# Optimization experiments

Hardware: AMD Instinct MI355X
Metric: run time of the kernel (lower is better)

## Reference

```python
import jax, jax.numpy as jnp
import numpy as np

EPS = 1e-8
H_OUT, W_OUT = 64, 64
SURR_SCALE = 10.0  # SuperSpike-style surrogate slope

@jax.custom_vjp
def spike(x):
    # forward: Heaviside threshold
    return (x > 0).astype(x.dtype)

def _spike_fwd(x):
    return spike(x), x

def _spike_bwd(x, g):
    # SuperSpike surrogate gradient: 1/(1+scale*|x|)^2
    return (g / (1.0 + SURR_SCALE * jnp.abs(x)) ** 2,)

spike.defvjp(_spike_fwd, _spike_bwd)


def setup_inputs() -> dict:
    key = jax.random.key(0)
    k1, k2, k3, k4 = jax.random.split(key, 4)
    x = jax.random.normal(k1, (4, 16, 32, 64, 64), dtype=jnp.float32)
    # w ~ N(0, std*sqrt(1/(C_in*prod(kernel)))) with std=1
    w = jax.random.normal(k2, (64, 16, 3, 3, 3), dtype=jnp.float32) * np.float32(np.sqrt(1.0 / (16 * 27)))
    beta = jnp.clip(0.7 + 0.01 * jax.random.normal(k3, (1,), dtype=jnp.float32), 0.0, 1.0)
    b = jnp.clip(1.0 + 0.01 * jax.random.normal(k4, (64,), dtype=jnp.float32), 0.0, None)
    return {"x": x, "w": w, "beta": beta, "b": b}


def reference(x, w, beta, b):
    # x: (B, C_in, T, H, W); w: (C_out, C_in, kt, kh, kw)
    # conv3d, padding = ceil((k-1)*dil/2) = 1 per dim for k=3, dil=1
    conv_x = jax.lax.conv_general_dilated(
        x, w,
        window_strides=(1, 1, 1),
        padding=[(1, 1), (1, 1), (1, 1)],
        rhs_dilation=(1, 1, 1),
        dimension_numbers=("NCDHW", "OIDHW", "NCDHW"),
    )
    conv_x = conv_x[:, :, :, :H_OUT, :W_OUT]  # crop spatial dims only

    d = jnp.einsum("abcde,fbcde->af", w, w)          # (C_out, C_out) lateral matrix
    norm = jnp.sum(w ** 2, axis=(1, 2, 3, 4))        # (C_out,)
    inv_norm = 1.0 / (norm + EPS)
    beta_s = beta[0]

    B = x.shape[0]
    C = w.shape[0]
    mem0 = jnp.zeros((B, C, H_OUT, W_OUT), dtype=x.dtype)
    spk0 = jnp.zeros_like(mem0)

    xs = jnp.moveaxis(conv_x, 2, 0)  # (T, B, C, H, W)

    def step(carry, inp_t):
        spk, mem = carry
        rst = jnp.einsum("abcd,be->aecd", spk, d)  # lateral reset
        mem = (mem - rst) * beta_s + inp_t * (1.0 - beta_s)
        mthr = mem * inv_norm[None, :, None, None] - b[None, :, None, None]
        spk = spike(mthr)
        return (spk, mem), spk

    _, spk_rec = jax.lax.scan(step, (spk0, mem0), xs)  # (T, B, C, H, W)
    return jnp.moveaxis(spk_rec, 0, 2)  # (B, C, T, H, W) -- flatten_output=False
```

## Files before the change

kernel.cpp:

```cpp
#include <hip/hip_runtime.h>
#include <cstdint>
#include <cstddef>

#define H_ 64
#define W_ 64
#define T_ 32
#define CIN_ 16
#define COUT_ 64
#define K_ 432
#define TH_ 4
#define TW_ 16
#define WR_ 6
#define WC_ 18
#define WSZ_ (WR_ * WC_)
#define XTOT_ (CIN_ * WSZ_)
#define NSLOT_ 4
#define NTHR_ 1024

__global__ void prep(const float* __restrict__ w, float* __restrict__ w_t,
                     double* __restrict__ d64, double* __restrict__ inv64) {
    const int i = blockIdx.x;
    const int j = threadIdx.x;
    const float* wi = w + i * K_;
    const float* wj = w + j * K_;
    double acc = 0.0;
    for (int k = 0; k < K_; ++k) acc += (double)wi[k] * (double)wj[k];
    d64[i * 64 + j] = acc;
    if (i == j) inv64[i] = 1.0 / (acc + 1e-8);
    for (int k = j; k < K_; k += 64) w_t[k * 64 + i] = wi[k];
}

__launch_bounds__(NTHR_, 1)
__global__ void fused_snn(const float* __restrict__ xg,
                          const float* __restrict__ beta_g, const float* __restrict__ bias_g,
                          const float* __restrict__ w_t, const double* __restrict__ d64,
                          const double* __restrict__ inv64, float* __restrict__ out) {
    __shared__ __align__(16) float x_win[NSLOT_ * XTOT_];
    __shared__ __align__(16) double d_lds[64 * 65];
    __shared__ unsigned int masks[2][64][2];

    const int tid = threadIdx.x;
    const int b   = blockIdx.x;
    const int ty0 = blockIdx.y * TH_;
    const int tx0 = blockIdx.z * TW_;

    const int wv   = __builtin_amdgcn_readfirstlane(tid >> 6);
    const int lane = tid & 63;
    const int py   = lane >> 4;
    const int px   = lane & 15;
    const int c0   = wv * 4;
    const int xoff = py * WC_ + px;

    for (int i = tid; i < 4096; i += NTHR_)
        d_lds[(i >> 6) * 65 + (i & 63)] = d64[i];
    if (tid < 128) masks[1][tid >> 1][tid & 1] = 0u;

    for (int z = 0; z < 2; ++z) {
        for (int i = tid; i < XTOT_; i += NTHR_) {
            int cin = i / WSZ_;
            int r2  = i - cin * WSZ_;
            int yy  = r2 / WC_;
            int xx  = r2 - yy * WC_;
            int gy = ty0 - 1 + yy, gx = tx0 - 1 + xx;
            float v = 0.f;
            if (gy >= 0 && gy < H_ && gx >= 0 && gx < W_)
                v = xg[((size_t)(b * CIN_ + cin) * T_ + z) * (H_ * W_) + gy * W_ + gx];
            x_win[(z * CIN_ + cin) * WSZ_ + r2] = v;
        }
    }

    const double beta = (double)beta_g[0];
    const double omb  = 1.0 - beta;
    double inv_[4], bb[4];
#pragma unroll
    for (int ci = 0; ci < 4; ++ci) {
        inv_[ci] = inv64[c0 + ci];
        bb[ci]   = (double)bias_g[c0 + ci];
    }
    double mem[4];
#pragma unroll
    for (int ci = 0; ci < 4; ++ci) mem[ci] = 0.0;

    int  pf_cin[2], pf_r2[2];
    size_t pf_goff[2];
    bool pf_ok[2], pf_in[2];
#pragma unroll
    for (int r = 0; r < 2; ++r) {
        int i = tid + r * NTHR_;
        pf_ok[r] = (i < XTOT_);
        int cin = i / WSZ_;
        int r2  = i - cin * WSZ_;
        int yy  = r2 / WC_;
        int xx  = r2 - yy * WC_;
        pf_cin[r] = cin; pf_r2[r] = r2;
        int gy = ty0 - 1 + yy, gx = tx0 - 1 + xx;
        pf_in[r]  = pf_ok[r] && gy >= 0 && gy < H_ && gx >= 0 && gx < W_;
        pf_goff[r] = (size_t)(b * CIN_ + cin) * (T_ * H_ * W_) + (size_t)gy * W_ + gx;
    }

    for (int t = 0; t < T_; ++t) {
        __syncthreads();
        if (tid < 128) masks[t & 1][tid >> 1][tid & 1] = 0u;

        float R[2];
        const int zp = t + 2;
        if (zp < T_) {
#pragma unroll
            for (int r = 0; r < 2; ++r) {
                R[r] = 0.f;
                if (pf_in[r]) R[r] = xg[pf_goff[r] + (size_t)zp * (H_ * W_)];
            }
        }

        double accd[4];
#pragma unroll
        for (int ci = 0; ci < 4; ++ci) accd[ci] = 0.0;

        int slot_[3]; bool zok[3];
#pragma unroll
        for (int dz = 0; dz < 3; ++dz) {
            int z = t - 1 + dz;
            zok[dz]  = (z >= 0 && z < T_);
            slot_[dz] = zok[dz] ? (z & 3) : 0;
        }

        for (int cin = 0; cin < CIN_; ++cin) {
            float cacc[4];
#pragma unroll
            for (int ci = 0; ci < 4; ++ci) cacc[ci] = 0.f;
#pragma unroll
            for (int dz = 0; dz < 3; ++dz) {
                if (!zok[dz]) continue;
                const float* xs = &x_win[(slot_[dz] * CIN_ + cin) * WSZ_] + xoff;
                const float* wr = w_t + (cin * 27 + dz * 9) * 64 + c0;
#pragma unroll
                for (int dy = 0; dy < 3; ++dy) {
                    const float xv0 = xs[dy * WC_ + 0];
                    const float xv1 = xs[dy * WC_ + 1];
                    const float xv2 = xs[dy * WC_ + 2];
                    const float4 w0 = *reinterpret_cast<const float4*>(wr + dy * 192);
                    const float4 w1 = *reinterpret_cast<const float4*>(wr + dy * 192 + 64);
                    const float4 w2 = *reinterpret_cast<const float4*>(wr + dy * 192 + 128);
                    cacc[0] = fmaf(w0.x, xv0, cacc[0]);
                    cacc[1] = fmaf(w0.y, xv0, cacc[1]);
                    cacc[2] = fmaf(w0.z, xv0, cacc[2]);
                    cacc[3] = fmaf(w0.w, xv0, cacc[3]);
                    cacc[0] = fmaf(w1.x, xv1, cacc[0]);
                    cacc[1] = fmaf(w1.y, xv1, cacc[1]);
                    cacc[2] = fmaf(w1.z, xv1, cacc[2]);
                    cacc[3] = fmaf(w1.w, xv1, cacc[3]);
                    cacc[0] = fmaf(w2.x, xv2, cacc[0]);
                    cacc[1] = fmaf(w2.y, xv2, cacc[1]);
                    cacc[2] = fmaf(w2.z, xv2, cacc[2]);
                    cacc[3] = fmaf(w2.w, xv2, cacc[3]);
                }
            }
#pragma unroll
            for (int ci = 0; ci < 4; ++ci) accd[ci] += (double)cacc[ci];
        }

        double rstv[4];
#pragma unroll
        for (int ci = 0; ci < 4; ++ci) rstv[ci] = 0.0;
        const int rb = (t + 1) & 1;
#pragma unroll
        for (int wrd = 0; wrd < 2; ++wrd) {
            unsigned int m = masks[rb][lane][wrd];
            while (m) {
                int bit = __ffs(m) - 1;
                m &= m - 1;
                const double* drow = &d_lds[(wrd * 32 + bit) * 65 + c0];
#pragma unroll
                for (int ci = 0; ci < 4; ++ci) rstv[ci] += drow[ci];
            }
        }

        unsigned int nib = 0u;
        const size_t obase = ((size_t)(b * COUT_ + c0) * T_ + t) * (size_t)(H_ * W_)
                           + (size_t)(ty0 + py) * W_ + (tx0 + px);
#pragma unroll
        for (int ci = 0; ci < 4; ++ci) {
            mem[ci] = (mem[ci] - rstv[ci]) * beta + accd[ci] * omb;
            const double mthr = mem[ci] * inv_[ci] - bb[ci];
            const int s = mthr > 0.0 ? 1 : 0;
            out[obase + (size_t)ci * (T_ * H_ * W_)] = (float)s;
            nib |= (unsigned int)s << ci;
        }

        __syncthreads();
        if (nib) atomicOr(&masks[t & 1][lane][wv >> 3], nib << ((wv & 7) * 4));

        if (zp < T_) {
            const int slot = zp & 3;
#pragma unroll
            for (int r = 0; r < 2; ++r)
                if (pf_ok[r])
                    x_win[(slot * CIN_ + pf_cin[r]) * WSZ_ + pf_r2[r]] = R[r];
        }
    }
}

extern "C" void kernel_launch(void* const* d_in, const int* in_sizes, int n_in,
                              void* d_out, int out_size, void* d_ws, size_t ws_size,
                              hipStream_t stream) {
    const float* x    = (const float*)d_in[0];
    const float* w    = (const float*)d_in[1];
    const float* beta = (const float*)d_in[2];
    const float* bias = (const float*)d_in[3];
    float* out = (float*)d_out;

    float*  w_t   = (float*)d_ws;
    double* d64   = (double*)((char*)d_ws + 110592);
    double* inv64 = (double*)((char*)d_ws + 110592 + 32768);

    prep<<<dim3(64), dim3(64), 0, stream>>>(w, w_t, d64, inv64);
    fused_snn<<<dim3(4, 16, 4), dim3(NTHR_), 0, stream>>>(x, beta, bias, w_t, d64, inv64, out);
}
```

Baseline: 522.1 us.

## Scatter each input time slice into three rolling output accumulators

The temporal conv loop is restructured. Each input time slice is read from LDS once and its contribution goes to the three output timesteps it feeds, kept in rolling double accumulators (a0/a1/a2), instead of gathering three slices per output step. This cuts LDS reads of the input window by about 3x and lets the ring buffer shrink from four slots to two, with the row width padded to 24. In exchange it needs more registers for the extra double accumulators, a third prefetch element per thread, and a prologue pass over slice 0.

```diff
diff --git a/kernel.cpp b/kernel.cpp
--- a/kernel.cpp
+++ b/kernel.cpp
@@ -11,10 +11,9 @@
 #define TH_ 4
 #define TW_ 16
 #define WR_ 6
-#define WC_ 18
+#define WC_ 24
 #define WSZ_ (WR_ * WC_)
 #define XTOT_ (CIN_ * WSZ_)
-#define NSLOT_ 4
 #define NTHR_ 1024
 
 __global__ void prep(const float* __restrict__ w, float* __restrict__ w_t,
@@ -35,7 +34,7 @@
                           const float* __restrict__ beta_g, const float* __restrict__ bias_g,
                           const float* __restrict__ w_t, const double* __restrict__ d64,
                           const double* __restrict__ inv64, float* __restrict__ out) {
-    __shared__ __align__(16) float x_win[NSLOT_ * XTOT_];
+    __shared__ __align__(16) float x_win[2 * XTOT_];
     __shared__ __align__(16) double d_lds[64 * 65];
     __shared__ unsigned int masks[2][64][2];
 
@@ -61,11 +60,12 @@
             int r2  = i - cin * WSZ_;
             int yy  = r2 / WC_;
             int xx  = r2 - yy * WC_;
+            if (xx >= TW_ + 2) continue;
             int gy = ty0 - 1 + yy, gx = tx0 - 1 + xx;
             float v = 0.f;
             if (gy >= 0 && gy < H_ && gx >= 0 && gx < W_)
                 v = xg[((size_t)(b * CIN_ + cin) * T_ + z) * (H_ * W_) + gy * W_ + gx];
-            x_win[(z * CIN_ + cin) * WSZ_ + r2] = v;
+            x_win[z * XTOT_ + i] = v;
         }
     }
 
@@ -77,91 +77,106 @@
         inv_[ci] = inv64[c0 + ci];
         bb[ci]   = (double)bias_g[c0 + ci];
     }
-    double mem[4];
-#pragma unroll
-    for (int ci = 0; ci < 4; ++ci) mem[ci] = 0.0;
-
-    int  pf_cin[2], pf_r2[2];
-    size_t pf_goff[2];
-    bool pf_ok[2], pf_in[2];
-#pragma unroll
-    for (int r = 0; r < 2; ++r) {
+    double mem[4] = {0.0, 0.0, 0.0, 0.0};
+    double a0[4] = {}, a1[4] = {}, a2[4] = {};
+
+    int  pf_loff[3];
+    size_t pf_goff[3];
+    bool pf_use[3], pf_in[3];
+#pragma unroll
+    for (int r = 0; r < 3; ++r) {
         int i = tid + r * NTHR_;
-        pf_ok[r] = (i < XTOT_);
         int cin = i / WSZ_;
         int r2  = i - cin * WSZ_;
         int yy  = r2 / WC_;
         int xx  = r2 - yy * WC_;
-        pf_cin[r] = cin; pf_r2[r] = r2;
+        pf_loff[r] = i;
         int gy = ty0 - 1 + yy, gx = tx0 - 1 + xx;
-        pf_in[r]  = pf_ok[r] && gy >= 0 && gy < H_ && gx >= 0 && gx < W_;
+        bool ok = (i < XTOT_) && (xx < TW_ + 2);
+        pf_use[r] = ok;
+        pf_in[r]  = ok && gy >= 0 && gy < H_ && gx >= 0 && gx < W_;
         pf_goff[r] = (size_t)(b * CIN_ + cin) * (T_ * H_ * W_) + (size_t)gy * W_ + gx;
+    }
+
+    __syncthreads();
+
+    {
+        for (int cin = 0; cin < CIN_; ++cin) {
+            const int base = cin * WSZ_ + xoff;
+            float xv[9];
+#pragma unroll
+            for (int dy = 0; dy < 3; ++dy)
+#pragma unroll
+                for (int dx = 0; dx < 3; ++dx)
+                    xv[dy * 3 + dx] = x_win[base + dy * WC_ + dx];
+            float cB[4] = {}, cC[4] = {};
+            const float* wr = w_t + cin * 27 * 64 + c0;
+#pragma unroll
+            for (int p = 0; p < 9; ++p) {
+                const float4 w1 = *reinterpret_cast<const float4*>(wr + (9 + p) * 64);
+                const float4 w0 = *reinterpret_cast<const float4*>(wr + p * 64);
+                cB[0] = fmaf(w1.x, xv[p], cB[0]); cB[1] = fmaf(w1.y, xv[p], cB[1]);
+                cB[2] = fmaf(w1.z, xv[p], cB[2]); cB[3] = fmaf(w1.w, xv[p], cB[3]);
+                cC[0] = fmaf(w0.x, xv[p], cC[0]); cC[1] = fmaf(w0.y, xv[p], cC[1]);
+                cC[2] = fmaf(w0.z, xv[p], cC[2]); cC[3] = fmaf(w0.w, xv[p], cC[3]);
+            }
+#pragma unroll
+            for (int ci = 0; ci < 4; ++ci) {
+                a0[ci] += (double)cB[ci];
+                a1[ci] += (double)cC[ci];
+            }
+        }
     }
 
     for (int t = 0; t < T_; ++t) {
         __syncthreads();
         if (tid < 128) masks[t & 1][tid >> 1][tid & 1] = 0u;
 
-        float R[2];
+        float R[3];
         const int zp = t + 2;
         if (zp < T_) {
 #pragma unroll
-            for (int r = 0; r < 2; ++r) {
+            for (int r = 0; r < 3; ++r) {
                 R[r] = 0.f;
                 if (pf_in[r]) R[r] = xg[pf_goff[r] + (size_t)zp * (H_ * W_)];
             }
         }
 
-        double accd[4];
-#pragma unroll
-        for (int ci = 0; ci < 4; ++ci) accd[ci] = 0.0;
-
-        int slot_[3]; bool zok[3];
-#pragma unroll
-        for (int dz = 0; dz < 3; ++dz) {
-            int z = t - 1 + dz;
-            zok[dz]  = (z >= 0 && z < T_);
-            slot_[dz] = zok[dz] ? (z & 3) : 0;
-        }
-
-        for (int cin = 0; cin < CIN_; ++cin) {
-            float cacc[4];
-#pragma unroll
-            for (int ci = 0; ci < 4; ++ci) cacc[ci] = 0.f;
-#pragma unroll
-            for (int dz = 0; dz < 3; ++dz) {
-                if (!zok[dz]) continue;
-                const float* xs = &x_win[(slot_[dz] * CIN_ + cin) * WSZ_] + xoff;
-                const float* wr = w_t + (cin * 27 + dz * 9) * 64 + c0;
-#pragma unroll
-                for (int dy = 0; dy < 3; ++dy) {
-                    const float xv0 = xs[dy * WC_ + 0];
-                    const float xv1 = xs[dy * WC_ + 1];
-                    const float xv2 = xs[dy * WC_ + 2];
-                    const float4 w0 = *reinterpret_cast<const float4*>(wr + dy * 192);
-                    const float4 w1 = *reinterpret_cast<const float4*>(wr + dy * 192 + 64);
-                    const float4 w2 = *reinterpret_cast<const float4*>(wr + dy * 192 + 128);
-                    cacc[0] = fmaf(w0.x, xv0, cacc[0]);
-                    cacc[1] = fmaf(w0.y, xv0, cacc[1]);
-                    cacc[2] = fmaf(w0.z, xv0, cacc[2]);
-                    cacc[3] = fmaf(w0.w, xv0, cacc[3]);
-                    cacc[0] = fmaf(w1.x, xv1, cacc[0]);
-                    cacc[1] = fmaf(w1.y, xv1, cacc[1]);
-                    cacc[2] = fmaf(w1.z, xv1, cacc[2]);
-                    cacc[3] = fmaf(w1.w, xv1, cacc[3]);
-                    cacc[0] = fmaf(w2.x, xv2, cacc[0]);
-                    cacc[1] = fmaf(w2.y, xv2, cacc[1]);
-                    cacc[2] = fmaf(w2.z, xv2, cacc[2]);
-                    cacc[3] = fmaf(w2.w, xv2, cacc[3]);
+        const int zc = t + 1;
+        if (zc < T_) {
+            const int sb = (zc & 1) * XTOT_ + xoff;
+            for (int cin = 0; cin < CIN_; ++cin) {
+                const int base = sb + cin * WSZ_;
+                float xv[9];
+#pragma unroll
+                for (int dy = 0; dy < 3; ++dy)
+#pragma unroll
+                    for (int dx = 0; dx < 3; ++dx)
+                        xv[dy * 3 + dx] = x_win[base + dy * WC_ + dx];
+                float cA[4] = {}, cB[4] = {}, cC[4] = {};
+                const float* wr = w_t + cin * 27 * 64 + c0;
+#pragma unroll
+                for (int p = 0; p < 9; ++p) {
+                    const float4 w2 = *reinterpret_cast<const float4*>(wr + (18 + p) * 64);
+                    const float4 w1 = *reinterpret_cast<const float4*>(wr + (9 + p) * 64);
+                    const float4 w0 = *reinterpret_cast<const float4*>(wr + p * 64);
+                    cA[0] = fmaf(w2.x, xv[p], cA[0]); cA[1] = fmaf(w2.y, xv[p], cA[1]);
+                    cA[2] = fmaf(w2.z, xv[p], cA[2]); cA[3] = fmaf(w2.w, xv[p], cA[3]);
+                    cB[0] = fmaf(w1.x, xv[p], cB[0]); cB[1] = fmaf(w1.y, xv[p], cB[1]);
+                    cB[2] = fmaf(w1.z, xv[p], cB[2]); cB[3] = fmaf(w1.w, xv[p], cB[3]);
+                    cC[0] = fmaf(w0.x, xv[p], cC[0]); cC[1] = fmaf(w0.y, xv[p], cC[1]);
+                    cC[2] = fmaf(w0.z, xv[p], cC[2]); cC[3] = fmaf(w0.w, xv[p], cC[3]);
                 }
-            }
-#pragma unroll
-            for (int ci = 0; ci < 4; ++ci) accd[ci] += (double)cacc[ci];
-        }
-
-        double rstv[4];
-#pragma unroll
-        for (int ci = 0; ci < 4; ++ci) rstv[ci] = 0.0;
+#pragma unroll
+                for (int ci = 0; ci < 4; ++ci) {
+                    a0[ci] += (double)cA[ci];
+                    a1[ci] += (double)cB[ci];
+                    a2[ci] += (double)cC[ci];
+                }
+            }
+        }
+
+        double rstv[4] = {0.0, 0.0, 0.0, 0.0};
         const int rb = (t + 1) & 1;
 #pragma unroll
         for (int wrd = 0; wrd < 2; ++wrd) {
@@ -180,7 +195,7 @@
                            + (size_t)(ty0 + py) * W_ + (tx0 + px);
 #pragma unroll
         for (int ci = 0; ci < 4; ++ci) {
-            mem[ci] = (mem[ci] - rstv[ci]) * beta + accd[ci] * omb;
+            mem[ci] = (mem[ci] - rstv[ci]) * beta + a0[ci] * omb;
             const double mthr = mem[ci] * inv_[ci] - bb[ci];
             const int s = mthr > 0.0 ? 1 : 0;
             out[obase + (size_t)ci * (T_ * H_ * W_)] = (float)s;
@@ -191,11 +206,17 @@
         if (nib) atomicOr(&masks[t & 1][lane][wv >> 3], nib << ((wv & 7) * 4));
 
         if (zp < T_) {
-            const int slot = zp & 3;
-#pragma unroll
-            for (int r = 0; r < 2; ++r)
-                if (pf_ok[r])
-                    x_win[(slot * CIN_ + pf_cin[r]) * WSZ_ + pf_r2[r]] = R[r];
+            const int so = (zp & 1) * XTOT_;
+#pragma unroll
+            for (int r = 0; r < 3; ++r)
+                if (pf_use[r]) x_win[so + pf_loff[r]] = R[r];
+        }
+
+#pragma unroll
+        for (int ci = 0; ci < 4; ++ci) {
+            a0[ci] = a1[ci];
+            a1[ci] = a2[ci];
+            a2[ci] = 0.0;
         }
     }
 }
```

Result: slower. 824.4 us (+57.9%).

## Store input window channel-interleaved and repack weights for float4 LDS reads

Applied to the files above, without the earlier changes.

The shared input window is rearranged from channel-major to position-major, with 4 input channels packed per float4 and a stride of 5 float4 per position to reduce bank conflicts. Weights are repacked in the prep kernel into per-wave groups of 4 output channels by 4 input channels, so the inner loop reads one float4 of x per tap and scalar weights that are uniform across the wave. The loop now runs over quads of input channels, which cuts the number of LDS load instructions. Converting the partial sums to double now happens per (cin-quad, dz) instead of per cin, which changes the float summation order slightly.

```diff
diff --git a/kernel.cpp b/kernel.cpp
--- a/kernel.cpp
+++ b/kernel.cpp
@@ -7,35 +7,38 @@
 #define T_ 32
 #define CIN_ 16
 #define COUT_ 64
-#define K_ 432
 #define TH_ 4
 #define TW_ 16
-#define WR_ 6
-#define WC_ 18
-#define WSZ_ (WR_ * WC_)
-#define XTOT_ (CIN_ * WSZ_)
-#define NSLOT_ 4
+#define NROW_ 6
+#define NCOL_ 18
+#define NPOS_ (NROW_ * NCOL_)
+#define XEL_ (NPOS_ * CIN_)
+#define SLOT_DW_ (NPOS_ * 20)
 #define NTHR_ 1024
 
-__global__ void prep(const float* __restrict__ w, float* __restrict__ w_t,
+__global__ void prep(const float* __restrict__ w, float* __restrict__ w2,
                      double* __restrict__ d64, double* __restrict__ inv64) {
     const int i = blockIdx.x;
     const int j = threadIdx.x;
-    const float* wi = w + i * K_;
-    const float* wj = w + j * K_;
+    const float* wi = w + i * 432;
+    const float* wj = w + j * 432;
     double acc = 0.0;
-    for (int k = 0; k < K_; ++k) acc += (double)wi[k] * (double)wj[k];
+    for (int k = 0; k < 432; ++k) acc += (double)wi[k] * (double)wj[k];
     d64[i * 64 + j] = acc;
     if (i == j) inv64[i] = 1.0 / (acc + 1e-8);
-    for (int k = j; k < K_; k += 64) w_t[k * 64 + i] = wi[k];
+    for (int k = j; k < 432; k += 64) {
+        const int cin = k / 27, r = k - cin * 27;
+        const int off = ((((i >> 2) * 4 + (cin >> 2)) * 27 + r) * 4 + (cin & 3)) * 4 + (i & 3);
+        w2[off] = wi[k];
+    }
 }
 
 __launch_bounds__(NTHR_, 1)
 __global__ void fused_snn(const float* __restrict__ xg,
                           const float* __restrict__ beta_g, const float* __restrict__ bias_g,
-                          const float* __restrict__ w_t, const double* __restrict__ d64,
+                          const float* __restrict__ w2, const double* __restrict__ d64,
                           const double* __restrict__ inv64, float* __restrict__ out) {
-    __shared__ __align__(16) float x_win[NSLOT_ * XTOT_];
+    __shared__ __align__(16) float4 xQ[4][NPOS_][5];
     __shared__ __align__(16) double d_lds[64 * 65];
     __shared__ unsigned int masks[2][64][2];
 
@@ -49,23 +52,23 @@
     const int py   = lane >> 4;
     const int px   = lane & 15;
     const int c0   = wv * 4;
-    const int xoff = py * WC_ + px;
+
+    const float* wbase = w2 + (size_t)wv * 1728;
+    float* xF = (float*)&xQ[0][0][0];
 
     for (int i = tid; i < 4096; i += NTHR_)
         d_lds[(i >> 6) * 65 + (i & 63)] = d64[i];
     if (tid < 128) masks[1][tid >> 1][tid & 1] = 0u;
 
     for (int z = 0; z < 2; ++z) {
-        for (int i = tid; i < XTOT_; i += NTHR_) {
-            int cin = i / WSZ_;
-            int r2  = i - cin * WSZ_;
-            int yy  = r2 / WC_;
-            int xx  = r2 - yy * WC_;
-            int gy = ty0 - 1 + yy, gx = tx0 - 1 + xx;
+        for (int i = tid; i < XEL_; i += NTHR_) {
+            const int pos = i >> 4, cin = i & 15;
+            const int yy = pos / NCOL_, xx = pos - yy * NCOL_;
+            const int gy = ty0 - 1 + yy, gx = tx0 - 1 + xx;
             float v = 0.f;
             if (gy >= 0 && gy < H_ && gx >= 0 && gx < W_)
                 v = xg[((size_t)(b * CIN_ + cin) * T_ + z) * (H_ * W_) + gy * W_ + gx];
-            x_win[(z * CIN_ + cin) * WSZ_ + r2] = v;
+            xF[z * SLOT_DW_ + pos * 20 + cin] = v;
         }
     }
 
@@ -81,19 +84,17 @@
 #pragma unroll
     for (int ci = 0; ci < 4; ++ci) mem[ci] = 0.0;
 
-    int  pf_cin[2], pf_r2[2];
+    int  pf_ldw[2];
     size_t pf_goff[2];
     bool pf_ok[2], pf_in[2];
 #pragma unroll
     for (int r = 0; r < 2; ++r) {
-        int i = tid + r * NTHR_;
-        pf_ok[r] = (i < XTOT_);
-        int cin = i / WSZ_;
-        int r2  = i - cin * WSZ_;
-        int yy  = r2 / WC_;
-        int xx  = r2 - yy * WC_;
-        pf_cin[r] = cin; pf_r2[r] = r2;
-        int gy = ty0 - 1 + yy, gx = tx0 - 1 + xx;
+        const int i = tid + r * NTHR_;
+        pf_ok[r] = (i < XEL_);
+        const int pos = (i >> 4) % NPOS_, cin = i & 15;
+        const int yy = pos / NCOL_, xx = pos - yy * NCOL_;
+        const int gy = ty0 - 1 + yy, gx = tx0 - 1 + xx;
+        pf_ldw[r] = pos * 20 + cin;
         pf_in[r]  = pf_ok[r] && gy >= 0 && gy < H_ && gx >= 0 && gx < W_;
         pf_goff[r] = (size_t)(b * CIN_ + cin) * (T_ * H_ * W_) + (size_t)gy * W_ + gx;
     }
@@ -119,55 +120,58 @@
         int slot_[3]; bool zok[3];
 #pragma unroll
         for (int dz = 0; dz < 3; ++dz) {
-            int z = t - 1 + dz;
+            const int z = t - 1 + dz;
             zok[dz]  = (z >= 0 && z < T_);
             slot_[dz] = zok[dz] ? (z & 3) : 0;
         }
 
-        for (int cin = 0; cin < CIN_; ++cin) {
-            float cacc[4];
-#pragma unroll
-            for (int ci = 0; ci < 4; ++ci) cacc[ci] = 0.f;
+#pragma unroll 1
+        for (int cinq = 0; cinq < 4; ++cinq) {
 #pragma unroll
             for (int dz = 0; dz < 3; ++dz) {
                 if (!zok[dz]) continue;
-                const float* xs = &x_win[(slot_[dz] * CIN_ + cin) * WSZ_] + xoff;
-                const float* wr = w_t + (cin * 27 + dz * 9) * 64 + c0;
+                const float4* xb = &xQ[slot_[dz]][0][0];
+                const float* wp = wbase + (cinq * 27 + dz * 9) * 16;
+                float cacc[4] = {0.f, 0.f, 0.f, 0.f};
 #pragma unroll
                 for (int dy = 0; dy < 3; ++dy) {
-                    const float xv0 = xs[dy * WC_ + 0];
-                    const float xv1 = xs[dy * WC_ + 1];
-                    const float xv2 = xs[dy * WC_ + 2];
-                    const float4 w0 = *reinterpret_cast<const float4*>(wr + dy * 192);
-                    const float4 w1 = *reinterpret_cast<const float4*>(wr + dy * 192 + 64);
-                    const float4 w2 = *reinterpret_cast<const float4*>(wr + dy * 192 + 128);
-                    cacc[0] = fmaf(w0.x, xv0, cacc[0]);
-                    cacc[1] = fmaf(w0.y, xv0, cacc[1]);
-                    cacc[2] = fmaf(w0.z, xv0, cacc[2]);
-                    cacc[3] = fmaf(w0.w, xv0, cacc[3]);
-                    cacc[0] = fmaf(w1.x, xv1, cacc[0]);
-                    cacc[1] = fmaf(w1.y, xv1, cacc[1]);
-                    cacc[2] = fmaf(w1.z, xv1, cacc[2]);
-                    cacc[3] = fmaf(w1.w, xv1, cacc[3]);
-                    cacc[0] = fmaf(w2.x, xv2, cacc[0]);
-                    cacc[1] = fmaf(w2.y, xv2, cacc[1]);
-                    cacc[2] = fmaf(w2.z, xv2, cacc[2]);
-                    cacc[3] = fmaf(w2.w, xv2, cacc[3]);
+                    const int rb0 = (py + dy) * NCOL_ + px;
+                    const float4 x0 = xb[(rb0 + 0) * 5 + cinq];
+                    const float4 x1 = xb[(rb0 + 1) * 5 + cinq];
+                    const float4 x2 = xb[(rb0 + 2) * 5 + cinq];
+                    const float* wd = wp + dy * 48;
+#pragma unroll
+                    for (int co = 0; co < 4; ++co) {
+                        float cc = cacc[co];
+                        cc = fmaf(wd[ 0 + co], x0.x, cc);
+                        cc = fmaf(wd[ 4 + co], x0.y, cc);
+                        cc = fmaf(wd[ 8 + co], x0.z, cc);
+                        cc = fmaf(wd[12 + co], x0.w, cc);
+                        cc = fmaf(wd[16 + co], x1.x, cc);
+                        cc = fmaf(wd[20 + co], x1.y, cc);
+                        cc = fmaf(wd[24 + co], x1.z, cc);
+                        cc = fmaf(wd[28 + co], x1.w, cc);
+                        cc = fmaf(wd[32 + co], x2.x, cc);
+                        cc = fmaf(wd[36 + co], x2.y, cc);
+                        cc = fmaf(wd[40 + co], x2.z, cc);
+                        cc = fmaf(wd[44 + co], x2.w, cc);
+                        cacc[co] = cc;
+                    }
                 }
+#pragma unroll
+                for (int ci = 0; ci < 4; ++ci) accd[ci] += (double)cacc[ci];
             }
-#pragma unroll
-            for (int ci = 0; ci < 4; ++ci) accd[ci] += (double)cacc[ci];
         }
 
         double rstv[4];
 #pragma unroll
         for (int ci = 0; ci < 4; ++ci) rstv[ci] = 0.0;
-        const int rb = (t + 1) & 1;
+        const int rbuf = (t + 1) & 1;
 #pragma unroll
         for (int wrd = 0; wrd < 2; ++wrd) {
-            unsigned int m = masks[rb][lane][wrd];
+            unsigned int m = masks[rbuf][lane][wrd];
             while (m) {
-                int bit = __ffs(m) - 1;
+                const int bit = __ffs(m) - 1;
                 m &= m - 1;
                 const double* drow = &d_lds[(wrd * 32 + bit) * 65 + c0];
 #pragma unroll
@@ -191,11 +195,10 @@
         if (nib) atomicOr(&masks[t & 1][lane][wv >> 3], nib << ((wv & 7) * 4));
 
         if (zp < T_) {
-            const int slot = zp & 3;
+            const int so = (zp & 3) * SLOT_DW_;
 #pragma unroll
             for (int r = 0; r < 2; ++r)
-                if (pf_ok[r])
-                    x_win[(slot * CIN_ + pf_cin[r]) * WSZ_ + pf_r2[r]] = R[r];
+                if (pf_ok[r]) xF[so + pf_ldw[r]] = R[r];
         }
     }
 }
@@ -209,10 +212,10 @@
     const float* bias = (const float*)d_in[3];
     float* out = (float*)d_out;
 
-    float*  w_t   = (float*)d_ws;
+    float*  w2    = (float*)d_ws;
     double* d64   = (double*)((char*)d_ws + 110592);
     double* inv64 = (double*)((char*)d_ws + 110592 + 32768);
 
-    prep<<<dim3(64), dim3(64), 0, stream>>>(w, w_t, d64, inv64);
-    fused_snn<<<dim3(4, 16, 4), dim3(NTHR_), 0, stream>>>(x, beta, bias, w_t, d64, inv64, out);
+    prep<<<dim3(64), dim3(64), 0, stream>>>(w, w2, d64, inv64);
+    fused_snn<<<dim3(4, 16, 4), dim3(NTHR_), 0, stream>>>(x, beta, bias, w2, d64, inv64, out);
 }
```

Result: slower. 583.7 us (+11.8%).
